# Kernel tuning notes

Hardware: AMD Instinct MI355X
Metric: run time of the kernel (lower is better)

## Reference

```python
import jax, jax.numpy as jnp
import numpy as np

C = 128


def _dw_conv(x, w, pad):
    # depthwise conv, NCHW, weight OIHW with I=1, groups=C
    return jax.lax.conv_general_dilated(
        x, w, window_strides=(1, 1), padding=pad,
        dimension_numbers=('NCHW', 'OIHW', 'NCHW'),
        feature_group_count=x.shape[1])


def _pw(x, w):
    # 1x1 conv as einsum; w: [O, I, 1, 1]
    return jnp.einsum('bihw,oi->bohw', x, w[:, :, 0, 0])


def _lrelu(x):
    return jax.nn.leaky_relu(x, 0.1)


def setup_inputs() -> dict:
    key = jax.random.key(0)
    ks = jax.random.split(key, 8)
    return {
        'x': jax.random.normal(ks[0], (2, C, 320, 320), dtype=jnp.float32),
        'w_h_dw': jax.random.normal(ks[1], (C, 1, 1, 5), dtype=jnp.float32) * 0.1,
        'w_h_pw': jax.random.normal(ks[2], (C, C, 1, 1), dtype=jnp.float32) * 0.05,
        'w_v_dw': jax.random.normal(ks[3], (C, 1, 5, 1), dtype=jnp.float32) * 0.1,
        'w_v_pw': jax.random.normal(ks[4], (C, C, 1, 1), dtype=jnp.float32) * 0.05,
        'w_dm1': jax.random.normal(ks[5], (C // 4, C, 1, 1), dtype=jnp.float32) * 0.05,
        'w_dm2': jax.random.normal(ks[6], (C, C // 4, 1, 1), dtype=jnp.float32) * 0.05,
        'w_fuse': jax.random.normal(ks[7], (C, 2 * C, 1, 1), dtype=jnp.float32) * 0.05,
        'scale': jnp.ones((1,), dtype=jnp.float32) * 0.3,
        'angRes': 5,
    }


def reference(x, w_h_dw, w_h_pw, w_v_dw, w_v_pw, w_dm1, w_dm2, w_fuse, scale, angRes):
    B, Cc, H, W = x.shape
    h, w = H // angRes, W // angRes
    # angular rearrange: [B,C,H,W] -> [B*h*w, C, angRes, angRes]
    xe = (x.reshape(B, Cc, h, angRes, w, angRes)
           .transpose(0, 2, 4, 1, 3, 5)
           .reshape(B * h * w, Cc, angRes, angRes))
    # horizontal EPI: depthwise 1x5 then 1x1
    eh = _pw(_lrelu(_dw_conv(xe, w_h_dw, ((0, 0), (2, 2)))), w_h_pw)
    # vertical EPI: depthwise 5x1 then 1x1
    ev = _pw(_lrelu(_dw_conv(xe, w_v_dw, ((2, 2), (0, 0)))), w_v_pw)

    def back(e):
        return (e.reshape(B, h, w, Cc, angRes, angRes)
                 .transpose(0, 3, 1, 4, 2, 5)
                 .reshape(B, Cc, H, W))

    eh, ev = back(eh), back(ev)
    epi = _pw(jnp.concatenate([eh, ev], axis=1), w_fuse)
    depth_w = jax.nn.sigmoid(_pw(_lrelu(_pw(epi, w_dm1)), w_dm2))
    return x + scale[0] * (epi * depth_w)
```

## Files before the change

### kernel.cpp

```cpp
#include <hip/hip_runtime.h>
#include <stdint.h>

typedef __bf16 bf16;
typedef __bf16 v8bf __attribute__((ext_vector_type(8)));
typedef __bf16 v4bf __attribute__((ext_vector_type(4)));
typedef float f32x4 __attribute__((ext_vector_type(4)));

#define MFMA16x16x32(a, b, c) __builtin_amdgcn_mfma_f32_16x16x32_bf16((a), (b), (c), 0, 0, 0)

__device__ __forceinline__ void async_ld16(const float* g, float* l) {
  __builtin_amdgcn_global_load_lds(
      (const __attribute__((address_space(1))) uint32_t*)g,
      (__attribute__((address_space(3))) uint32_t*)l, 16, 0, 0);
}

__global__ __launch_bounds__(64) void prep_wt(const float* __restrict__ wfuse,
                                              const float* __restrict__ whpw,
                                              const float* __restrict__ wvpw,
                                              bf16* __restrict__ Wt) {
  int id = blockIdx.x * 64 + threadIdx.x;
  int o = id >> 8, k = id & 255;
  int k7 = k & 127, kk = k7 >> 4, sl = k7 & 15, sub = sl >> 3, e = sl & 7;
  int ki = kk * 16 + (e + (e & 4)) + sub * 4;
  const float* fr = wfuse + o * 256 + (k < 128 ? 0 : 128);
  const float* pw = (k < 128) ? whpw : wvpw;
  float a0 = 0.f, a1 = 0.f, a2 = 0.f, a3 = 0.f;
#pragma unroll 8
  for (int j = 0; j < 128; j += 4) {
    a0 = fmaf(fr[j + 0], pw[(j + 0) * 128 + ki], a0);
    a1 = fmaf(fr[j + 1], pw[(j + 1) * 128 + ki], a1);
    a2 = fmaf(fr[j + 2], pw[(j + 2) * 128 + ki], a2);
    a3 = fmaf(fr[j + 3], pw[(j + 3) * 128 + ki], a3);
  }
  Wt[o * 256 + k] = (bf16)((a0 + a1) + (a2 + a3));
}

__global__ void prep_dm(const float* __restrict__ wdm1,
                        const float* __restrict__ wdm2,
                        bf16* __restrict__ W1, bf16* __restrict__ W2) {
  int id = blockIdx.x * 256 + threadIdx.x;
  if (id < 4096) W1[id] = (bf16)wdm1[id];
  else           W2[id - 4096] = (bf16)wdm2[id - 4096];
}

__global__ __launch_bounds__(512, 4) void fused_main(
    const float* __restrict__ x,
    const float* __restrict__ whdw,
    const float* __restrict__ wvdw,
    const bf16* __restrict__ Wt,
    const bf16* __restrict__ W1,
    const bf16* __restrict__ W2,
    const float* __restrict__ scalep,
    float* __restrict__ out) {
  __shared__ __align__(16) char smemc[81920];
  float* xs0 = (float*)smemc;
  float* xs1 = (float*)(smemc + 13056);
  float* whs = (float*)(smemc + 26112);
  float* wvs = (float*)(smemc + 32288);

  const int tid = threadIdx.x;
  const int w = tid >> 6, lane = tid & 63, ln16 = lane & 15, q = lane >> 4;
  const int hv = q >> 1;
  const int csel = (q & 1) * 4;
  const bool has1 = (w <= 4);

  const int bx = blockIdx.x;
  const int wc = bx & 7, hi = (bx >> 3) & 63, b = bx >> 9;
  const size_t xbase = (size_t)b * 13107200 + (size_t)(hi * 5) * 320 + (size_t)(wc * 40);
  const float* gx = x + xbase;

  for (int i = tid; i < 1280; i += 512) {
    int j = (i < 640) ? i : (i - 640);
    int c = j / 5, t = j - c * 5;
    float v = (i < 640) ? whdw[j] : wvdw[j];
    ((i < 640) ? whs : wvs)[c * 12 + t] = v;
  }
  if (tid < 128) {
    float* bufp = (tid & 64) ? xs1 : xs0;
    int c = (tid & 63) >> 2, p = tid & 3;
    bufp[c * 204 + 200 + p] = 0.f;
  }

  int pk[2];
#pragma unroll
  for (int s = 0; s < 2; ++s) {
    int pos = (w + 8 * s) * 16 + ln16;
    if (pos > 199) pos = 199;
    int a = pos / 40;
    int col = pos - a * 40;
    int aw = col - (col / 5) * 5;
    pk[s] = a | (col << 8) | (aw << 16);
  }

  auto stage = [&](int kk, float* buf) {
    const int c0k = kk * 16;
#pragma unroll
    for (int h2 = 0; h2 < 2; ++h2) {
      const int c = w + 8 * h2;
      const float* gc = gx + (size_t)(c0k + c) * 102400;
      float* lb = buf + c * 204;
      if (lane < 50) {
        int r = lane / 10, c4 = lane - r * 10;
        async_ld16(gc + r * 320 + c4 * 4, lb);
      }
    }
  };

  f32x4 acc[2][8];
#pragma unroll
  for (int s = 0; s < 2; ++s)
#pragma unroll
    for (int m = 0; m < 8; ++m) acc[s][m] = (f32x4){0.f, 0.f, 0.f, 0.f};

  stage(0, xs0);

  for (int kk = 0; kk < 8; ++kk) {
    float* cur = (kk & 1) ? xs1 : xs0;
    float* nxt = (kk & 1) ? xs0 : xs1;
    const int c0 = kk * 16;
    __syncthreads();

    if (kk < 7) stage(kk + 1, nxt);

    const float* wbase = (hv ? wvs : whs) + c0 * 12;
    v8bf bvs[2];
#pragma unroll
    for (int s = 0; s < 2; ++s) {
      if (s == 1 && !has1) break;
      const int a = pk[s] & 255, col = (pk[s] >> 8) & 255, aw = pk[s] >> 16;
      const int base = a * 40 + col;
      int tap[5];
#pragma unroll
      for (int t = 0; t < 5; ++t) {
        const int d = t - 2;
        const int th = ((unsigned)(aw + d) < 5u) ? (base + d) : 200;
        const int tv = ((unsigned)(a + d) < 5u) ? (base + d * 40) : 200;
        tap[t] = hv ? tv : th;
      }
#pragma unroll 4
      for (int c = 0; c < 8; ++c) {
        const int ch = c + (c & 4) + csel;
        const float4 wv4 = *(const float4*)(wbase + ch * 12);
        const float w4v = wbase[ch * 12 + 4];
        const float* xp = cur + ch * 204;
        float d = wv4.x * xp[tap[0]];
        d = fmaf(wv4.y, xp[tap[1]], d);
        d = fmaf(wv4.z, xp[tap[2]], d);
        d = fmaf(wv4.w, xp[tap[3]], d);
        d = fmaf(w4v, xp[tap[4]], d);
        d = fmaxf(d, 0.f) + 0.1f * fminf(d, 0.f);
        bvs[s][c] = (bf16)d;
      }
    }

    v8bf af[8];
    const int koff = c0 + (q & 1) * 8 + hv * 128;
#pragma unroll
    for (int m = 0; m < 8; ++m)
      af[m] = *(const v8bf*)(Wt + (m * 16 + ln16) * 256 + koff);
#pragma unroll
    for (int m = 0; m < 8; ++m)
      acc[0][m] = MFMA16x16x32(af[m], bvs[0], acc[0][m]);
    if (has1) {
#pragma unroll
      for (int m = 0; m < 8; ++m)
        acc[1][m] = MFMA16x16x32(af[m], bvs[1], acc[1][m]);
    }
  }
  __syncthreads();

  char* wreg = smemc + w * 10240;
  bf16* es = (bf16*)wreg;
  bf16* ts = es;
  float* con = (float*)wreg;
  const float scl = scalep[0];
#define ESI(row, colv) ((row) * 144 + ((colv) ^ (((row) & 7) << 3)))

#pragma unroll
  for (int s = 0; s < 2; ++s) {
    const int nt = w + 8 * s;
    if (nt <= 12) {
#pragma unroll
      for (int m = 0; m < 8; ++m) {
        v4bf v;
        v[0] = (bf16)acc[s][m][0];
        v[1] = (bf16)acc[s][m][1];
        v[2] = (bf16)acc[s][m][2];
        v[3] = (bf16)acc[s][m][3];
        *(v4bf*)(es + ESI(ln16, m * 16 + q * 4)) = v;
      }
      f32x4 tacc[2];
      tacc[0] = (f32x4){0.f, 0.f, 0.f, 0.f};
      tacc[1] = (f32x4){0.f, 0.f, 0.f, 0.f};
#pragma unroll
      for (int ks = 0; ks < 4; ++ks) {
        v8bf bfr = *(const v8bf*)(es + ESI(ln16, ks * 32 + q * 8));
#pragma unroll
        for (int m2 = 0; m2 < 2; ++m2) {
          v8bf afr = *(const v8bf*)(W1 + (m2 * 16 + ln16) * 128 + ks * 32 + q * 8);
          tacc[m2] = MFMA16x16x32(afr, bfr, tacc[m2]);
        }
      }
#pragma unroll
      for (int m2 = 0; m2 < 2; ++m2) {
        v4bf v;
#pragma unroll
        for (int r = 0; r < 4; ++r) {
          float tv = tacc[m2][r];
          tv = fmaxf(tv, 0.f) + 0.1f * fminf(tv, 0.f);
          v[r] = (bf16)tv;
        }
        *(v4bf*)(ts + ln16 * 40 + m2 * 16 + q * 4) = v;
      }
      v8bf tb = *(const v8bf*)(ts + ln16 * 40 + q * 8);
#pragma unroll
      for (int m = 0; m < 8; ++m) {
        v8bf afr2 = *(const v8bf*)(W2 + (m * 16 + ln16) * 32 + q * 8);
        f32x4 z = {0.f, 0.f, 0.f, 0.f};
        f32x4 dacc = MFMA16x16x32(afr2, tb, z);
#pragma unroll
        for (int r = 0; r < 4; ++r) {
          const float sig = 1.0f / (1.0f + __expf(-dacc[r]));
          con[(m * 16 + q * 4 + r) * 20 + ln16] = scl * acc[s][m][r] * sig;
        }
      }
      const int ol = lane >> 2;
      const int p4 = (lane & 3) * 4;
      const int pos = nt * 16 + p4;
      if (pos < 200) {
        const int a = pos / 40, colp = pos - a * 40;
        const size_t rowoff = xbase + (size_t)(a * 320 + colp);
#pragma unroll
        for (int i = 0; i < 8; ++i) {
          const int oo = i * 16 + ol;
          const f32x4 c4 = *(const f32x4*)(con + oo * 20 + p4);
          const size_t g = rowoff + (size_t)oo * 102400;
          const float4 xv = *(const float4*)(x + g);
          float4 ov;
          ov.x = xv.x + c4[0];
          ov.y = xv.y + c4[1];
          ov.z = xv.z + c4[2];
          ov.w = xv.w + c4[3];
          *(float4*)(out + g) = ov;
        }
      }
    }
  }
#undef ESI
}

extern "C" void kernel_launch(void* const* d_in, const int* in_sizes, int n_in,
                              void* d_out, int out_size, void* d_ws, size_t ws_size,
                              hipStream_t stream) {
  (void)in_sizes; (void)n_in; (void)out_size; (void)ws_size;
  const float* x     = (const float*)d_in[0];
  const float* whdw  = (const float*)d_in[1];
  const float* whpw  = (const float*)d_in[2];
  const float* wvdw  = (const float*)d_in[3];
  const float* wvpw  = (const float*)d_in[4];
  const float* wdm1  = (const float*)d_in[5];
  const float* wdm2  = (const float*)d_in[6];
  const float* wfuse = (const float*)d_in[7];
  const float* scale = (const float*)d_in[8];

  bf16* Wt = (bf16*)d_ws;
  bf16* W1 = Wt + 32768;
  bf16* W2 = W1 + 4096;

  prep_wt<<<512, 64, 0, stream>>>(wfuse, whpw, wvpw, Wt);
  prep_dm<<<32, 256, 0, stream>>>(wdm1, wdm2, W1, W2);
  fused_main<<<1024, 512, 0, stream>>>(x, whdw, wvdw, Wt, W1, W2, scale, (float*)d_out);
}
```

Measured before the change: 342.5 us.

## Precompute depthwise stencil into LDS staging buffers and software-pipeline with MFMA

Replaces the per-lane 5-tap depthwise stencil, which computed each output with scattered LDS reads inside the MFMA loop, with a cooperative stencil pass. Each thread loads one 5-element row or column once and produces all 5 outputs, writing bf16 results into double-buffered LDS staging in the layout the MFMA B operand expects. The loop becomes a three-stage pipeline: the async global load runs two chunks ahead, the stencil one chunk ahead, and MFMA consumes the current staged chunk. This removes redundant tap loads and the boundary index logic, and the simpler K layout lets prep_wt drop its permutation. In exchange it uses more LDS for the staging buffers and a deeper prologue.

```diff
diff --git a/kernel.cpp b/kernel.cpp
--- a/kernel.cpp
+++ b/kernel.cpp
@@ -19,9 +19,7 @@
                                               const float* __restrict__ wvpw,
                                               bf16* __restrict__ Wt) {
   int id = blockIdx.x * 64 + threadIdx.x;
-  int o = id >> 8, k = id & 255;
-  int k7 = k & 127, kk = k7 >> 4, sl = k7 & 15, sub = sl >> 3, e = sl & 7;
-  int ki = kk * 16 + (e + (e & 4)) + sub * 4;
+  int o = id >> 8, k = id & 255, ki = k & 127;
   const float* fr = wfuse + o * 256 + (k < 128 ? 0 : 128);
   const float* pw = (k < 128) ? whpw : wvpw;
   float a0 = 0.f, a1 = 0.f, a2 = 0.f, a3 = 0.f;
@@ -55,13 +53,14 @@
   __shared__ __align__(16) char smemc[81920];
   float* xs0 = (float*)smemc;
   float* xs1 = (float*)(smemc + 13056);
-  float* whs = (float*)(smemc + 26112);
-  float* wvs = (float*)(smemc + 32288);
+  char* st0c = smemc + 26112;
+  char* st1c = smemc + 39424;
+  float* whs = (float*)(smemc + 52736);
+  float* wvs = (float*)(smemc + 56832);
 
   const int tid = threadIdx.x;
   const int w = tid >> 6, lane = tid & 63, ln16 = lane & 15, q = lane >> 4;
   const int hv = q >> 1;
-  const int csel = (q & 1) * 4;
   const bool has1 = (w <= 4);
 
   const int bx = blockIdx.x;
@@ -73,24 +72,72 @@
     int j = (i < 640) ? i : (i - 640);
     int c = j / 5, t = j - c * 5;
     float v = (i < 640) ? whdw[j] : wvdw[j];
-    ((i < 640) ? whs : wvs)[c * 12 + t] = v;
-  }
-  if (tid < 128) {
-    float* bufp = (tid & 64) ? xs1 : xs0;
-    int c = (tid & 63) >> 2, p = tid & 3;
-    bufp[c * 204 + 200 + p] = 0.f;
-  }
-
-  int pk[2];
-#pragma unroll
-  for (int s = 0; s < 2; ++s) {
-    int pos = (w + 8 * s) * 16 + ln16;
-    if (pos > 199) pos = 199;
-    int a = pos / 40;
-    int col = pos - a * 40;
-    int aw = col - (col / 5) * 5;
-    pk[s] = a | (col << 8) | (aw << 16);
-  }
+    ((i < 640) ? whs : wvs)[c * 8 + t] = v;
+  }
+  if (tid < 256) {
+    int bsel = tid >> 7, rem = tid & 127;
+    int orient = rem >> 6, rr = rem & 63;
+    int pos = 200 + (rr >> 3), chp = rr & 7;
+    *(uint32_t*)((bsel ? st1c : st0c) + orient * 6656 + pos * 32 + chp * 4) = 0u;
+  }
+
+  int xidx0, stf0, ch0, hvt0;
+  int xidx1, stf1, ch1, hvt1;
+  int xidx2, stf2, ch2, hvt2;
+  {
+    int T = tid;
+    int c = T & 15, tI = T >> 4;
+    int base = (tI >> 3) * 40 + (tI & 7) * 5;
+    xidx0 = c * 204 + base; stf0 = base * 32 + c * 2; ch0 = c; hvt0 = 0;
+  }
+  {
+    int T = tid + 512;
+    int iv = (T >= 640) ? 1 : 0;
+    int r = T - (iv ? 640 : 0);
+    int c = r & 15, tI = r >> 4;
+    int base = iv ? tI : ((tI >> 3) * 40 + (tI & 7) * 5);
+    xidx1 = c * 204 + base; stf1 = iv * 6656 + base * 32 + c * 2; ch1 = c; hvt1 = iv;
+  }
+  {
+    int T = tid + 1024;
+    int r = T - 640;
+    int c = r & 15, tI = r >> 4;
+    xidx2 = c * 204 + tI; stf2 = 6656 + tI * 32 + c * 2; ch2 = c; hvt2 = 1;
+  }
+
+  const int boff0 = hv * 6656 + (w * 16 + ln16) * 32 + (q & 1) * 16;
+  const int boff1 = hv * 6656 + ((w + 8) * 16 + ln16) * 32 + (q & 1) * 16;
+
+  auto run_task = [&](const float* xb, char* stb, int c0,
+                      int xidx, int stoff, int ch, int ishv) {
+    const float* wrow = (ishv ? wvs : whs) + (c0 + ch) * 8;
+    const float4 wv = *(const float4*)wrow;
+    const float w4 = wrow[4];
+    const float* xq = xb + xidx;
+    float x0, x1, x2, x3, x4;
+    if (ishv) { x0 = xq[0]; x1 = xq[40]; x2 = xq[80]; x3 = xq[120]; x4 = xq[160]; }
+    else      { x0 = xq[0]; x1 = xq[1];  x2 = xq[2];  x3 = xq[3];   x4 = xq[4]; }
+    float o0 = fmaf(w4, x2, fmaf(wv.w, x1, wv.z * x0));
+    float o1 = fmaf(w4, x3, fmaf(wv.w, x2, fmaf(wv.z, x1, wv.y * x0)));
+    float o2 = fmaf(w4, x4, fmaf(wv.w, x3, fmaf(wv.z, x2, fmaf(wv.y, x1, wv.x * x0))));
+    float o3 = fmaf(wv.w, x4, fmaf(wv.z, x3, fmaf(wv.y, x2, wv.x * x1)));
+    float o4 = fmaf(wv.z, x4, fmaf(wv.y, x3, wv.x * x2));
+    auto lr = [](float v) { return fmaxf(v, 0.f) + 0.1f * fminf(v, 0.f); };
+    bf16* sp = (bf16*)(stb + stoff);
+    if (ishv) {
+      sp[0]    = (bf16)lr(o0); sp[640]  = (bf16)lr(o1); sp[1280] = (bf16)lr(o2);
+      sp[1920] = (bf16)lr(o3); sp[2560] = (bf16)lr(o4);
+    } else {
+      sp[0]  = (bf16)lr(o0); sp[16] = (bf16)lr(o1); sp[32] = (bf16)lr(o2);
+      sp[48] = (bf16)lr(o3); sp[64] = (bf16)lr(o4);
+    }
+  };
+
+  auto do_stencil = [&](int c0, const float* xb, char* stb) {
+    run_task(xb, stb, c0, xidx0, stf0, ch0, hvt0);
+    run_task(xb, stb, c0, xidx1, stf1, ch1, hvt1);
+    if (tid < 256) run_task(xb, stb, c0, xidx2, stf2, ch2, hvt2);
+  };
 
   auto stage = [&](int kk, float* buf) {
     const int c0k = kk * 16;
@@ -113,61 +160,33 @@
     for (int m = 0; m < 8; ++m) acc[s][m] = (f32x4){0.f, 0.f, 0.f, 0.f};
 
   stage(0, xs0);
+  stage(1, xs1);
+  __syncthreads();
+  do_stencil(0, xs0, st0c);
+  __syncthreads();
 
   for (int kk = 0; kk < 8; ++kk) {
-    float* cur = (kk & 1) ? xs1 : xs0;
-    float* nxt = (kk & 1) ? xs0 : xs1;
-    const int c0 = kk * 16;
-    __syncthreads();
-
-    if (kk < 7) stage(kk + 1, nxt);
-
-    const float* wbase = (hv ? wvs : whs) + c0 * 12;
-    v8bf bvs[2];
-#pragma unroll
-    for (int s = 0; s < 2; ++s) {
-      if (s == 1 && !has1) break;
-      const int a = pk[s] & 255, col = (pk[s] >> 8) & 255, aw = pk[s] >> 16;
-      const int base = a * 40 + col;
-      int tap[5];
-#pragma unroll
-      for (int t = 0; t < 5; ++t) {
-        const int d = t - 2;
-        const int th = ((unsigned)(aw + d) < 5u) ? (base + d) : 200;
-        const int tv = ((unsigned)(a + d) < 5u) ? (base + d * 40) : 200;
-        tap[t] = hv ? tv : th;
-      }
-#pragma unroll 4
-      for (int c = 0; c < 8; ++c) {
-        const int ch = c + (c & 4) + csel;
-        const float4 wv4 = *(const float4*)(wbase + ch * 12);
-        const float w4v = wbase[ch * 12 + 4];
-        const float* xp = cur + ch * 204;
-        float d = wv4.x * xp[tap[0]];
-        d = fmaf(wv4.y, xp[tap[1]], d);
-        d = fmaf(wv4.z, xp[tap[2]], d);
-        d = fmaf(wv4.w, xp[tap[3]], d);
-        d = fmaf(w4v, xp[tap[4]], d);
-        d = fmaxf(d, 0.f) + 0.1f * fminf(d, 0.f);
-        bvs[s][c] = (bf16)d;
-      }
-    }
-
+    if (kk < 6) stage(kk + 2, (kk & 1) ? xs1 : xs0);
+    if (kk < 7) do_stencil((kk + 1) * 16, (kk & 1) ? xs0 : xs1,
+                           (kk & 1) ? st0c : st1c);
+    const char* stc = (kk & 1) ? st1c : st0c;
+    v8bf b0 = *(const v8bf*)(stc + boff0);
+    v8bf b1 = *(const v8bf*)(stc + boff1);
+    const int koff = kk * 16 + (q & 1) * 8 + hv * 128;
     v8bf af[8];
-    const int koff = c0 + (q & 1) * 8 + hv * 128;
 #pragma unroll
     for (int m = 0; m < 8; ++m)
       af[m] = *(const v8bf*)(Wt + (m * 16 + ln16) * 256 + koff);
 #pragma unroll
     for (int m = 0; m < 8; ++m)
-      acc[0][m] = MFMA16x16x32(af[m], bvs[0], acc[0][m]);
+      acc[0][m] = MFMA16x16x32(af[m], b0, acc[0][m]);
     if (has1) {
 #pragma unroll
       for (int m = 0; m < 8; ++m)
-        acc[1][m] = MFMA16x16x32(af[m], bvs[1], acc[1][m]);
-    }
-  }
-  __syncthreads();
+        acc[1][m] = MFMA16x16x32(af[m], b1, acc[1][m]);
+    }
+    __syncthreads();
+  }
 
   char* wreg = smemc + w * 10240;
   bf16* es = (bf16*)wreg;
```

Measured after the change: 348.2 us. Within noise of the previous version (+1.7%).
